# Performance work log

Measured on AMD Instinct MI355X. Metric: run time of the kernel, lower is better.

## Reference

```python
import jax, jax.numpy as jnp
import numpy as np

SIZE = 40  # region window (40, 40)
HALF = SIZE // 2


def setup_inputs() -> dict:
    B, H, W, K = 32, 1024, 1024, 4
    key = jax.random.key(0)
    preds = jax.random.uniform(key, (B, 1, H, W), dtype=jnp.float32)
    # deterministic blob centroids (y, x); one near the border to exercise clipping
    rng = np.random.default_rng(0)
    base = np.array([[200, 200], [200, 700], [700, 200], [30, 900]], dtype=np.int64)
    cents = np.zeros((B, K, 2), dtype=np.int32)
    gt = np.zeros((B, 1, H, W), dtype=np.float32)
    for b in range(B):
        jit = rng.integers(-50, 50, size=(K, 2))
        c = np.clip(base + jit, 5, H - 6)
        cents[b] = c
        for k in range(K):
            y, x = int(c[k, 0]), int(c[k, 1])
            gt[b, 0, y - 4:y + 5, x - 4:x + 5] = 1.0  # 9x9 blob -> centroid = (y, x)
    return {"preds": preds, "gt_masks": jnp.asarray(gt), "centroids": jnp.asarray(cents)}


def _bounds(c, dim):
    # replicates extract_region clipping + parity adjustment for fixed 40x40 window
    start = jnp.maximum(c - HALF, 0)
    end = jnp.minimum(c + HALF, dim)
    new = end - start
    odd_small = ((new % 2) != 0) & (new < SIZE)
    end = jnp.where(odd_small & (start == 0), end - 1, end)
    start = jnp.where(odd_small & (end == dim), start + 1, start)
    return start, end


def _region_iou_per_image(P, G, cent):
    # P, G: [H, W]; cent: [K, 2] (y, x) -> mean soft-IoU over K regions
    H, W = P.shape
    sy, ey = _bounds(cent[:, 0], H)   # [K]
    sx, ex = _bounds(cent[:, 1], W)
    ry = jnp.arange(H)
    rx = jnp.arange(W)
    row = ((ry[None, :] >= sy[:, None]) & (ry[None, :] < ey[:, None])).astype(P.dtype)  # [K,H]
    col = ((rx[None, :] >= sx[:, None]) & (rx[None, :] < ex[:, None])).astype(P.dtype)  # [K,W]
    inter = jnp.einsum('kh,hw,kw->k', row, P * G, col)
    psum = jnp.einsum('kh,hw,kw->k', row, P, col)
    gsum = jnp.einsum('kh,hw,kw->k', row, G, col)
    iou = (inter + 1.0) / (psum + gsum - inter + 1.0)
    return jnp.mean(iou)


def reference(preds, gt_masks, centroids):
    smooth = 1.0
    inter = jnp.sum(preds * gt_masks)
    loss_global = 1.0 - (inter + smooth) / (jnp.sum(preds) + jnp.sum(gt_masks) - inter + smooth)
    per_img = jax.vmap(_region_iou_per_image)(preds[:, 0], gt_masks[:, 0], centroids)  # [B]
    loss_region = 1.0 - jnp.mean(per_img)
    return loss_global + loss_region
```

## Files before the change

kernel.cpp:

```cpp
#include <hip/hip_runtime.h>

#define BATCH 32
#define HGT   1024
#define WID   1024
#define KREG  4
#define HALF  20

#define SUM_BLOCKS 4096
#define SUM_THREADS 256
#define UNROLL 8

__device__ __forceinline__ float wave_reduce_f(float v) {
    #pragma unroll
    for (int off = 32; off > 0; off >>= 1)
        v += __shfl_down(v, off, 64);
    return v;
}

__device__ __forceinline__ double wave_reduce_d(double v) {
    #pragma unroll
    for (int off = 32; off > 0; off >>= 1)
        v += __shfl_down(v, off, 64);
    return v;
}

__global__ __launch_bounds__(SUM_THREADS) void global_sums_kernel(
        const float4* __restrict__ p, const float4* __restrict__ g,
        float* __restrict__ part) {
    const long stride = (long)SUM_BLOCKS * SUM_THREADS;
    const long base   = (long)blockIdx.x * SUM_THREADS + threadIdx.x;

    float4 a[UNROLL], b[UNROLL];
    #pragma unroll
    for (int j = 0; j < UNROLL; ++j) a[j] = p[base + (long)j * stride];
    #pragma unroll
    for (int j = 0; j < UNROLL; ++j) b[j] = g[base + (long)j * stride];

    __syncthreads();

    float sp = 0.f, sg = 0.f, spg = 0.f;
    #pragma unroll
    for (int j = 0; j < UNROLL; ++j) {
        sp  += (a[j].x + a[j].y) + (a[j].z + a[j].w);
        sg  += (b[j].x + b[j].y) + (b[j].z + b[j].w);
        spg += (a[j].x * b[j].x + a[j].y * b[j].y)
             + (a[j].z * b[j].z + a[j].w * b[j].w);
    }

    spg = wave_reduce_f(spg);
    sp  = wave_reduce_f(sp);
    sg  = wave_reduce_f(sg);

    __shared__ float smem[3][4];
    int lane = threadIdx.x & 63;
    int wv   = threadIdx.x >> 6;
    if (lane == 0) { smem[0][wv] = spg; smem[1][wv] = sp; smem[2][wv] = sg; }
    __syncthreads();
    if (threadIdx.x == 0) {
        float tpg = 0.f, tp = 0.f, tg = 0.f;
        #pragma unroll
        for (int w = 0; w < SUM_THREADS / 64; ++w) {
            tpg += smem[0][w]; tp += smem[1][w]; tg += smem[2][w];
        }
        part[blockIdx.x]                  = tpg;
        part[SUM_BLOCKS + blockIdx.x]     = tp;
        part[2 * SUM_BLOCKS + blockIdx.x] = tg;
    }
}

__device__ __forceinline__ void region_bounds(int c, int dim, int& s, int& e) {
    s = max(c - HALF, 0);
    e = min(c + HALF, dim);
    int n = e - s;
    bool odd_small = ((n & 1) != 0) && (n < 2 * HALF);
    if (odd_small && s == 0) e -= 1;
    if (odd_small && e == dim) s += 1;
}

__global__ __launch_bounds__(256) void region_iou_kernel(
        const float* __restrict__ p, const float* __restrict__ g,
        const int* __restrict__ cents, float* __restrict__ ious) {
    int r = blockIdx.x;
    int b = r / KREG;
    int cy = cents[r * 2 + 0];
    int cx = cents[r * 2 + 1];

    int sy, ey, sx, ex;
    region_bounds(cy, HGT, sy, ey);
    region_bounds(cx, WID, sx, ex);
    int w = ex - sx;

    const float* pb = p + (size_t)b * HGT * WID;
    const float* gb = g + (size_t)b * HGT * WID;

    int lane = threadIdx.x & 63;
    int wv   = threadIdx.x >> 6;

    float sp = 0.f, sg = 0.f, spg = 0.f;
    if (lane < w) {
        for (int yy = sy + wv; yy < ey; yy += 4) {
            size_t off = (size_t)yy * WID + sx + lane;
            float pv = pb[off];
            float gv = gb[off];
            sp  += pv;
            sg  += gv;
            spg += pv * gv;
        }
    }
    spg = wave_reduce_f(spg);
    sp  = wave_reduce_f(sp);
    sg  = wave_reduce_f(sg);

    __shared__ float smem[3][4];
    if (lane == 0) { smem[0][wv] = spg; smem[1][wv] = sp; smem[2][wv] = sg; }
    __syncthreads();
    if (threadIdx.x == 0) {
        float tpg = 0.f, tp = 0.f, tg = 0.f;
        #pragma unroll
        for (int w2 = 0; w2 < 4; ++w2) {
            tpg += smem[0][w2]; tp += smem[1][w2]; tg += smem[2][w2];
        }
        ious[r] = (tpg + 1.0f) / (tp + tg - tpg + 1.0f);
    }
}

__global__ __launch_bounds__(256) void finalize_kernel(
        const float4* __restrict__ part4, const float* __restrict__ ious,
        float* __restrict__ out) {
    const int Q = SUM_BLOCKS / 4;
    double spg = 0.0, sp = 0.0, sg = 0.0, siou = 0.0;
    for (int i = threadIdx.x; i < Q; i += 256) {
        float4 v0 = part4[i];
        float4 v1 = part4[Q + i];
        float4 v2 = part4[2 * Q + i];
        spg += (double)((v0.x + v0.y) + (v0.z + v0.w));
        sp  += (double)((v1.x + v1.y) + (v1.z + v1.w));
        sg  += (double)((v2.x + v2.y) + (v2.z + v2.w));
    }
    if (threadIdx.x < BATCH * KREG) siou = (double)ious[threadIdx.x];

    spg  = wave_reduce_d(spg);
    sp   = wave_reduce_d(sp);
    sg   = wave_reduce_d(sg);
    siou = wave_reduce_d(siou);

    __shared__ double smem[4][4];
    int lane = threadIdx.x & 63;
    int wv   = threadIdx.x >> 6;
    if (lane == 0) {
        smem[0][wv] = spg; smem[1][wv] = sp; smem[2][wv] = sg; smem[3][wv] = siou;
    }
    __syncthreads();
    if (threadIdx.x == 0) {
        double tpg = 0.0, tp = 0.0, tg = 0.0, ti = 0.0;
        #pragma unroll
        for (int w = 0; w < 4; ++w) {
            tpg += smem[0][w]; tp += smem[1][w]; tg += smem[2][w]; ti += smem[3][w];
        }
        double loss_global = 1.0 - (tpg + 1.0) / (tp + tg - tpg + 1.0);
        double loss_region = 1.0 - ti / (double)(BATCH * KREG);
        out[0] = (float)(loss_global + loss_region);
    }
}

extern "C" void kernel_launch(void* const* d_in, const int* in_sizes, int n_in,
                              void* d_out, int out_size, void* d_ws, size_t ws_size,
                              hipStream_t stream) {
    const float* preds = (const float*)d_in[0];
    const float* gt    = (const float*)d_in[1];
    const int*   cents = (const int*)d_in[2];
    float* out = (float*)d_out;

    float* part = (float*)d_ws;
    float* ious = part + 3 * SUM_BLOCKS;

    global_sums_kernel<<<SUM_BLOCKS, SUM_THREADS, 0, stream>>>(
        (const float4*)preds, (const float4*)gt, part);
    region_iou_kernel<<<BATCH * KREG, 256, 0, stream>>>(preds, gt, cents, ious);
    finalize_kernel<<<1, 256, 0, stream>>>((const float4*)part, ious, out);
}
```

Baseline: 288.7 us.

## Split global sums into nontemporal-load half and cached half

Splits the global reduction into two kernels. The first half of the data is read with nontemporal loads so it does not pollute the cache. The second half, read last with normal loads, can stay resident in cache so the region IoU kernel may hit cache on windows located there. It also drops the needless __syncthreads after the loads. The cost is an extra kernel launch and a serialization point between the two halves.

```diff
diff --git a/kernel.cpp b/kernel.cpp
--- a/kernel.cpp
+++ b/kernel.cpp
@@ -7,8 +7,11 @@
 #define HALF  20
 
 #define SUM_BLOCKS 4096
+#define HALF_BLOCKS (SUM_BLOCKS / 2)
 #define SUM_THREADS 256
 #define UNROLL 8
+
+typedef float f32x4 __attribute__((ext_vector_type(4)));
 
 __device__ __forceinline__ float wave_reduce_f(float v) {
     #pragma unroll
@@ -24,33 +27,11 @@
     return v;
 }
 
-__global__ __launch_bounds__(SUM_THREADS) void global_sums_kernel(
-        const float4* __restrict__ p, const float4* __restrict__ g,
-        float* __restrict__ part) {
-    const long stride = (long)SUM_BLOCKS * SUM_THREADS;
-    const long base   = (long)blockIdx.x * SUM_THREADS + threadIdx.x;
-
-    float4 a[UNROLL], b[UNROLL];
-    #pragma unroll
-    for (int j = 0; j < UNROLL; ++j) a[j] = p[base + (long)j * stride];
-    #pragma unroll
-    for (int j = 0; j < UNROLL; ++j) b[j] = g[base + (long)j * stride];
-
-    __syncthreads();
-
-    float sp = 0.f, sg = 0.f, spg = 0.f;
-    #pragma unroll
-    for (int j = 0; j < UNROLL; ++j) {
-        sp  += (a[j].x + a[j].y) + (a[j].z + a[j].w);
-        sg  += (b[j].x + b[j].y) + (b[j].z + b[j].w);
-        spg += (a[j].x * b[j].x + a[j].y * b[j].y)
-             + (a[j].z * b[j].z + a[j].w * b[j].w);
-    }
-
+__device__ __forceinline__ void block_reduce_store(
+        float spg, float sp, float sg, float* __restrict__ part, int slot) {
     spg = wave_reduce_f(spg);
     sp  = wave_reduce_f(sp);
     sg  = wave_reduce_f(sg);
-
     __shared__ float smem[3][4];
     int lane = threadIdx.x & 63;
     int wv   = threadIdx.x >> 6;
@@ -62,10 +43,59 @@
         for (int w = 0; w < SUM_THREADS / 64; ++w) {
             tpg += smem[0][w]; tp += smem[1][w]; tg += smem[2][w];
         }
-        part[blockIdx.x]                  = tpg;
-        part[SUM_BLOCKS + blockIdx.x]     = tp;
-        part[2 * SUM_BLOCKS + blockIdx.x] = tg;
-    }
+        part[slot]                  = tpg;
+        part[SUM_BLOCKS + slot]     = tp;
+        part[2 * SUM_BLOCKS + slot] = tg;
+    }
+}
+
+__global__ __launch_bounds__(SUM_THREADS) void global_sums_nt_kernel(
+        const f32x4* __restrict__ p, const f32x4* __restrict__ g,
+        float* __restrict__ part) {
+    const long stride = (long)HALF_BLOCKS * SUM_THREADS;
+    const long base   = (long)blockIdx.x * SUM_THREADS + threadIdx.x;
+
+    f32x4 a[UNROLL], b[UNROLL];
+    #pragma unroll
+    for (int j = 0; j < UNROLL; ++j)
+        a[j] = __builtin_nontemporal_load(&p[base + (long)j * stride]);
+    #pragma unroll
+    for (int j = 0; j < UNROLL; ++j)
+        b[j] = __builtin_nontemporal_load(&g[base + (long)j * stride]);
+
+    float sp = 0.f, sg = 0.f, spg = 0.f;
+    #pragma unroll
+    for (int j = 0; j < UNROLL; ++j) {
+        sp  += (a[j].x + a[j].y) + (a[j].z + a[j].w);
+        sg  += (b[j].x + b[j].y) + (b[j].z + b[j].w);
+        spg += (a[j].x * b[j].x + a[j].y * b[j].y)
+             + (a[j].z * b[j].z + a[j].w * b[j].w);
+    }
+    block_reduce_store(spg, sp, sg, part, blockIdx.x);
+}
+
+__global__ __launch_bounds__(SUM_THREADS) void global_sums_reg_kernel(
+        const f32x4* __restrict__ p, const f32x4* __restrict__ g,
+        float* __restrict__ part) {
+    const long stride = (long)HALF_BLOCKS * SUM_THREADS;
+    const long half_off = (long)HALF_BLOCKS * SUM_THREADS * UNROLL;
+    const long base   = half_off + (long)blockIdx.x * SUM_THREADS + threadIdx.x;
+
+    f32x4 a[UNROLL], b[UNROLL];
+    #pragma unroll
+    for (int j = 0; j < UNROLL; ++j) a[j] = p[base + (long)j * stride];
+    #pragma unroll
+    for (int j = 0; j < UNROLL; ++j) b[j] = g[base + (long)j * stride];
+
+    float sp = 0.f, sg = 0.f, spg = 0.f;
+    #pragma unroll
+    for (int j = 0; j < UNROLL; ++j) {
+        sp  += (a[j].x + a[j].y) + (a[j].z + a[j].w);
+        sg  += (b[j].x + b[j].y) + (b[j].z + b[j].w);
+        spg += (a[j].x * b[j].x + a[j].y * b[j].y)
+             + (a[j].z * b[j].z + a[j].w * b[j].w);
+    }
+    block_reduce_store(spg, sp, sg, part, HALF_BLOCKS + blockIdx.x);
 }
 
 __device__ __forceinline__ void region_bounds(int c, int dim, int& s, int& e) {
@@ -174,8 +204,10 @@
     float* part = (float*)d_ws;
     float* ious = part + 3 * SUM_BLOCKS;
 
-    global_sums_kernel<<<SUM_BLOCKS, SUM_THREADS, 0, stream>>>(
-        (const float4*)preds, (const float4*)gt, part);
+    global_sums_nt_kernel<<<HALF_BLOCKS, SUM_THREADS, 0, stream>>>(
+        (const f32x4*)preds, (const f32x4*)gt, part);
+    global_sums_reg_kernel<<<HALF_BLOCKS, SUM_THREADS, 0, stream>>>(
+        (const f32x4*)preds, (const f32x4*)gt, part);
     region_iou_kernel<<<BATCH * KREG, 256, 0, stream>>>(preds, gt, cents, ious);
     finalize_kernel<<<1, 256, 0, stream>>>((const float4*)part, ious, out);
 }
```

Measured after the change: 275.9 us. 4.4% less time.
